# Kernel optimization log

Hardware: AMD Instinct MI355X
Metric: run time of the kernel (lower is better)

Reference implementation:

```python
import jax, jax.numpy as jnp
import numpy as np

B, N, Z = 32, 8192, 1024


def setup_inputs() -> dict:
    key = jax.random.key(0)
    ks = jax.random.split(key, 11)
    def w(k, shape, fan_in):
        # kaiming-ish init scale for conv1d k=1
        return jax.random.normal(k, shape, dtype=jnp.float32) * (1.0 / np.sqrt(fan_in))
    return {
        "x": jax.random.normal(ks[0], (B, 3, N), dtype=jnp.float32),
        "W1": w(ks[1], (64, 3), 3),   "b1": jnp.zeros((64,), jnp.float32),
        "W2": w(ks[2], (128, 64), 64), "b2": jnp.zeros((128,), jnp.float32),
        "W3": w(ks[3], (256, 128), 128), "b3": jnp.zeros((256,), jnp.float32),
        "W4": w(ks[4], (256, 256), 256), "b4": jnp.zeros((256,), jnp.float32),
        "W5": w(ks[5], (Z, 256), 256),  "b5": jnp.zeros((Z,), jnp.float32),
    }


def _pointwise(x, W, b):
    # Conv1d with kernel_size=1 == per-point linear: [B,C,N] x [O,C] -> [B,O,N]
    return jnp.einsum('bcn,oc->bon', x, W) + b[None, :, None]


def reference(x, W1, b1, W2, b2, W3, b3, W4, b4, W5, b5):
    h = jax.nn.relu(_pointwise(x, W1, b1))
    h = jax.nn.relu(_pointwise(h, W2, b2))
    h = jax.nn.relu(_pointwise(h, W3, b3))
    h = jax.nn.relu(_pointwise(h, W4, b4))
    h = _pointwise(h, W5, b5)           # [B, Z, N]
    return jnp.max(h, axis=2)           # global max pool over points -> [B, Z]
```

## Files before the change

### kernel.cpp

```cpp
#include <hip/hip_runtime.h>
#include <math.h>

#define NB      32
#define NPTS    8192
#define TOTPTS  (NB * NPTS)

typedef unsigned short u16;
typedef unsigned int   u32;
typedef __attribute__((ext_vector_type(8))) short bf16x8;
typedef __attribute__((ext_vector_type(4))) float f32x4;

__device__ __forceinline__ u16 f2bf(float f) {
    u32 u = __float_as_uint(f);
    u = (u + 0x7fffu + ((u >> 16) & 1u)) >> 16;
    return (u16)u;
}
__device__ __forceinline__ u32 pk2(float a, float b) {
    return (u32)f2bf(a) | ((u32)f2bf(b) << 16);
}
__device__ __forceinline__ f32x4 MFMA(bf16x8 a, bf16x8 b, f32x4 c) {
    return __builtin_amdgcn_mfma_f32_16x16x32_bf16(a, b, c, 0, 0, 0);
}
template<int CTRL>
__device__ __forceinline__ float dpp_max(float v) {
    int t = __builtin_amdgcn_update_dpp(__float_as_int(v), __float_as_int(v),
                                        CTRL, 0xF, 0xF, false);
    return fmaxf(v, __int_as_float(t));
}
__device__ __forceinline__ float rowmax16(float v) {
    v = dpp_max<0xB1>(v);
    v = dpp_max<0x4E>(v);
    v = dpp_max<0x141>(v);
    v = dpp_max<0x140>(v);
    return v;
}
__device__ __forceinline__ void gload16(const void* g, void* l) {
    __builtin_amdgcn_global_load_lds(
        (const __attribute__((address_space(1))) unsigned int*)g,
        (__attribute__((address_space(3))) unsigned int*)l, 16, 0, 0);
}
template<int N> __device__ __forceinline__ void vwait() {
    if constexpr (N == 0) asm volatile("s_waitcnt vmcnt(0)" ::: "memory");
    else                  asm volatile("s_waitcnt vmcnt(4)" ::: "memory");
}
__device__ __forceinline__ void pin(bf16x8& v)  { asm volatile("" : "+v"(v)); }
__device__ __forceinline__ void pinA(bf16x8& v) { asm volatile("" : "+a"(v)); }


__global__ __launch_bounds__(256) void k_pack(const float* __restrict__ W2,
        const float* __restrict__ W3, const float* __restrict__ W4,
        const float* __restrict__ W5, u16* __restrict__ dst) {
    int idx = blockIdx.x * 256 + threadIdx.x;
    if (idx >= 720 * 64) return;
    int lane = idx & 63, fr = idx >> 6;
    const float* W; int C, frl;
    if (fr < 16)       { W = W2; C = 64;  frl = fr;       }
    else if (fr < 80)  { W = W3; C = 128; frl = fr - 16;  }
    else if (fr < 208) { W = W4; C = 256; frl = fr - 80;  }
    else               { W = W5; C = 256; frl = fr - 208; }
    int KF = C >> 5;
    int nf = frl / KF, kf = frl % KF;
    int o = nf * 16 + (lane & 15), c = kf * 32 + (lane >> 4) * 8;
    const float* s = W + (size_t)o * C + c;
    u32 out[4];
    #pragma unroll
    for (int j = 0; j < 4; ++j) out[j] = pk2(s[2 * j], s[2 * j + 1]);
    *(uint4*)((char*)dst + (size_t)idx * 16) = make_uint4(out[0], out[1], out[2], out[3]);
}

__global__ __launch_bounds__(512, 2) void k_fuse(const float* __restrict__ x,
        const float* __restrict__ W1, const float* __restrict__ b1,
        const u16* __restrict__ W2p, const float* __restrict__ b2,
        const u16* __restrict__ W3p, const float* __restrict__ b3,
        const u16* __restrict__ W4p, const float* __restrict__ b4,
        u16* __restrict__ H4, int pt0, int tpb) {
    __shared__ char regA[65536];
    __shared__ char regB[32768];
    const int tid = threadIdx.x, lane = tid & 63, w = tid >> 6;
    const int l15 = lane & 15, q = lane >> 4;
    const int qterm = ((q >> 1) * 16 + l15) * 16 + (q & 1) * 8;
    const int pl = tid & 127;
    const int c4 = tid >> 7;

    bf16x8 W2r[2], W3r[2][4], W4r[2][8];
    #pragma unroll
    for (int kf = 0; kf < 2; ++kf) {
        W2r[kf] = *(const bf16x8*)((const char*)W2p + (size_t)(w * 2 + kf) * 1024 + lane * 16);
        pin(W2r[kf]);
    }
    #pragma unroll
    for (int n = 0; n < 2; ++n)
        #pragma unroll
        for (int kf = 0; kf < 4; ++kf) {
            W3r[n][kf] = *(const bf16x8*)((const char*)W3p +
                           (size_t)((w * 2 + n) * 4 + kf) * 1024 + lane * 16);
            pin(W3r[n][kf]);
        }
    #pragma unroll
    for (int n = 0; n < 2; ++n)
        #pragma unroll
        for (int kf = 0; kf < 8; ++kf) {
            W4r[n][kf] = *(const bf16x8*)((const char*)W4p +
                           (size_t)((w * 2 + n) * 8 + kf) * 1024 + lane * 16);
            pin(W4r[n][kf]);
        }
    const f32x4 b2v = *(const f32x4*)(b2 + w * 16 + q * 4);
    f32x4 b3v[2], b4v[2];
    #pragma unroll
    for (int n = 0; n < 2; ++n) {
        b3v[n] = *(const f32x4*)(b3 + (w * 2 + n) * 16 + q * 4);
        b4v[n] = *(const f32x4*)(b4 + (w * 2 + n) * 16 + q * 4);
    }

    const int tile0 = blockIdx.x * tpb;
    float x0, x1, x2;
    {
        int ptg = pt0 + tile0 * 128 + pl;
        const float* xb = x + (size_t)(ptg >> 13) * 3 * NPTS + (ptg & 8191);
        x0 = xb[0]; x1 = xb[NPTS]; x2 = xb[2 * NPTS];
    }

    for (int it = 0; it < tpb; ++it) {
        const int tile = tile0 + it;
        {
            u32 pk4[8];
            #pragma unroll
            for (int i = 0; i < 8; ++i) {
                int o0 = c4 * 16 + 2 * i, o1 = o0 + 1;
                float a0 = fmaxf(b1[o0] + W1[o0*3]*x0 + W1[o0*3+1]*x1 + W1[o0*3+2]*x2, 0.f);
                float a1 = fmaxf(b1[o1] + W1[o1*3]*x0 + W1[o1*3+1]*x1 + W1[o1*3+2]*x2, 0.f);
                pk4[i] = pk2(a0, a1);
            }
            char* rowp = regA + pl * 128;
            const int swz = (pl & 7) << 4;
            *(uint4*)(rowp + ((c4 * 32) ^ swz))      = make_uint4(pk4[0], pk4[1], pk4[2], pk4[3]);
            *(uint4*)(rowp + ((c4 * 32 + 16) ^ swz)) = make_uint4(pk4[4], pk4[5], pk4[6], pk4[7]);
        }
        __syncthreads();
        #pragma unroll
        for (int pf = 0; pf < 8; ++pf) {
            const int r2 = pf * 16 + l15;
            const char* rb = regA + r2 * 128;
            const int rsw = (r2 & 7) << 4;
            bf16x8 B0 = *(const bf16x8*)(rb + ((q * 16) ^ rsw));
            bf16x8 B1 = *(const bf16x8*)(rb + ((64 + q * 16) ^ rsw));
            f32x4 a = b2v;
            a = MFMA(W2r[0], B0, a);
            a = MFMA(W2r[1], B1, a);
            u32 d0 = pk2(fmaxf(a[0], 0.f), fmaxf(a[1], 0.f));
            u32 d1 = pk2(fmaxf(a[2], 0.f), fmaxf(a[3], 0.f));
            *(uint2*)(regB + (pf * 4 + (w >> 1)) * 1024 + (w & 1) * 512 + qterm)
                = make_uint2(d0, d1);
        }
        __syncthreads();
        #pragma unroll
        for (int pf = 0; pf < 8; ++pf) {
            bf16x8 B[4];
            #pragma unroll
            for (int kf = 0; kf < 4; ++kf)
                B[kf] = *(const bf16x8*)(regB + (pf * 4 + kf) * 1024 + lane * 16);
            f32x4 a0 = b3v[0], a1 = b3v[1];
            #pragma unroll
            for (int kf = 0; kf < 4; ++kf) {
                a0 = MFMA(W3r[0][kf], B[kf], a0);
                a1 = MFMA(W3r[1][kf], B[kf], a1);
            }
            char* db = regA + (pf * 8 + w) * 1024;
            *(uint2*)(db + qterm)       = make_uint2(pk2(fmaxf(a0[0],0.f), fmaxf(a0[1],0.f)),
                                                     pk2(fmaxf(a0[2],0.f), fmaxf(a0[3],0.f)));
            *(uint2*)(db + 512 + qterm) = make_uint2(pk2(fmaxf(a1[0],0.f), fmaxf(a1[1],0.f)),
                                                     pk2(fmaxf(a1[2],0.f), fmaxf(a1[3],0.f)));
        }
        __syncthreads();
        #pragma unroll
        for (int pf = 0; pf < 8; ++pf) {
            bf16x8 B[8];
            #pragma unroll
            for (int kf = 0; kf < 8; ++kf)
                B[kf] = *(const bf16x8*)(regA + (pf * 8 + kf) * 1024 + lane * 16);
            f32x4 a0 = b4v[0], a1 = b4v[1];
            #pragma unroll
            for (int kf = 0; kf < 8; ++kf) {
                a0 = MFMA(W4r[0][kf], B[kf], a0);
                a1 = MFMA(W4r[1][kf], B[kf], a1);
            }
            char* db = (char*)H4 + ((size_t)(tile * 8 + pf) * 8 + w) * 1024;
            *(uint2*)(db + qterm)       = make_uint2(pk2(fmaxf(a0[0],0.f), fmaxf(a0[1],0.f)),
                                                     pk2(fmaxf(a0[2],0.f), fmaxf(a0[3],0.f)));
            *(uint2*)(db + 512 + qterm) = make_uint2(pk2(fmaxf(a1[0],0.f), fmaxf(a1[1],0.f)),
                                                     pk2(fmaxf(a1[2],0.f), fmaxf(a1[3],0.f)));
        }
        if (it + 1 < tpb) {
            int ptg = pt0 + (tile + 1) * 128 + pl;
            const float* xb = x + (size_t)(ptg >> 13) * 3 * NPTS + (ptg & 8191);
            x0 = xb[0]; x1 = xb[NPTS]; x2 = xb[2 * NPTS];
        }
        __syncthreads();
    }
}

__global__ __launch_bounds__(512, 2) void k_l5(const u16* __restrict__ Hin,
        const u16* __restrict__ Wp, const float* __restrict__ b5,
        float* __restrict__ parts, int slot0) {
    constexpr int BUFB = 32768;
    constexpr int STEPS = 16;
    __shared__ char ldsB[2 * BUFB];
    const int tid = threadIdx.x, lane = tid & 63, w = tid >> 6;
    const int l15 = lane & 15, q = lane >> 4;
    const int zsl = blockIdx.x & 1, pgrp = blockIdx.x >> 1;
    const int pfb = pgrp * 64;

    bf16x8 W[4][8];
    {
        const char* wb = (const char*)Wp + (size_t)(zsl * 32 + w * 4) * 8 * 1024;
        #pragma unroll
        for (int nf = 0; nf < 4; ++nf)
            #pragma unroll
            for (int kf = 0; kf < 8; ++kf)
                W[nf][kf] = *(const bf16x8*)(wb + (size_t)(nf * 8 + kf) * 1024 + lane * 16);
    }
    f32x4 vmax[4];
    #pragma unroll
    for (int nf = 0; nf < 4; ++nf)
        #pragma unroll
        for (int r = 0; r < 4; ++r) vmax[nf][r] = -3.402823466e38f;

    auto stage = [&](int t, int bsel) {
        const char* g = (const char*)Hin + ((size_t)(pfb + t * 4) * 8) * 1024
                        + w * 4096 + lane * 16;
        char* l = ldsB + bsel * BUFB + w * 4096;
        gload16(g,        l);
        gload16(g + 1024, l + 1024);
        gload16(g + 2048, l + 2048);
        gload16(g + 3072, l + 3072);
    };
    stage(0, 0);
    for (int t = 0; t < STEPS; ++t) {
        vwait<0>();
        __builtin_amdgcn_sched_barrier(0);
        __builtin_amdgcn_s_barrier();
        if (t + 1 < STEPS) stage(t + 1, (t + 1) & 1);
        const char* bp = ldsB + (t & 1) * BUFB;
        #pragma unroll
        for (int p = 0; p < 4; ++p) {
            const int pe = (p + w) & 3;
            f32x4 acc[4];
            #pragma unroll
            for (int nf = 0; nf < 4; ++nf)
                #pragma unroll
                for (int r = 0; r < 4; ++r) acc[nf][r] = 0.f;
            #pragma unroll
            for (int kf = 0; kf < 8; ++kf) {
                bf16x8 B = *(const bf16x8*)(bp + (size_t)(pe * 8 + kf) * 1024 + lane * 16);
                #pragma unroll
                for (int nf = 0; nf < 4; ++nf) acc[nf] = MFMA(W[nf][kf], B, acc[nf]);
            }
            #pragma unroll
            for (int nf = 0; nf < 4; ++nf)
                #pragma unroll
                for (int r = 0; r < 4; ++r)
                    vmax[nf][r] = fmaxf(vmax[nf][r], acc[nf][r]);
        }
    }
    const int zb = zsl * 512 + w * 64;
    float* dst = parts + (size_t)(slot0 + pgrp) * 1024 + zb;
    #pragma unroll
    for (int nf = 0; nf < 4; ++nf)
        #pragma unroll
        for (int r = 0; r < 4; ++r) {
            float m = rowmax16(vmax[nf][r]);
            if (l15 == nf * 4 + r) {
                int zi = nf * 16 + q * 4 + r;
                dst[zi] = m + b5[zb + zi];
            }
        }
}

__global__ __launch_bounds__(256) void k_red(const float* __restrict__ parts,
                                             float* __restrict__ out) {
    int i = blockIdx.x * 256 + threadIdx.x;
    int b = i >> 10, z = i & 1023;
    float m = -3.402823466e38f;
    #pragma unroll
    for (int s = 0; s < 8; ++s)
        m = fmaxf(m, parts[((size_t)b * 8 + s) * 1024 + z]);
    out[i] = m;
}

extern "C" void kernel_launch(void* const* d_in, const int* in_sizes, int n_in,
                              void* d_out, int out_size, void* d_ws, size_t ws_size,
                              hipStream_t stream) {
    const float* x  = (const float*)d_in[0];
    const float* W1 = (const float*)d_in[1]; const float* b1 = (const float*)d_in[2];
    const float* W2 = (const float*)d_in[3]; const float* b2 = (const float*)d_in[4];
    const float* W3 = (const float*)d_in[5]; const float* b3 = (const float*)d_in[6];
    const float* W4 = (const float*)d_in[7]; const float* b4 = (const float*)d_in[8];
    const float* W5 = (const float*)d_in[9]; const float* b5 = (const float*)d_in[10];

    u16* wsW = (u16*)d_ws;
    const u16* W2p = (const u16*)((char*)d_ws + 0);
    const u16* W3p = (const u16*)((char*)d_ws + 16 * 1024);
    const u16* W4p = (const u16*)((char*)d_ws + 80 * 1024);
    const u16* W5p = (const u16*)((char*)d_ws + 208 * 1024);
    float* parts   = (float*)((char*)d_ws + 786432);
    char* Hbase    = (char*)d_ws + 786432 + 2097152;

    int NCH = 1;
    while (NCH < 32) {
        size_t npc = (size_t)TOTPTS / NCH;
        if (786432 + 2097152 + npc * 512 <= ws_size) break;
        NCH *= 2;
    }
    const size_t npts_c = (size_t)TOTPTS / NCH;
    char* HB = Hbase;

    k_pack<<<dim3(180), dim3(256), 0, stream>>>(W2, W3, W4, W5, wsW);

    const int ntiles = (int)(npts_c / 128);
    const int nblk   = (ntiles >= 256) ? 256 : ntiles;
    const int tpb    = ntiles / nblk;
    for (int c = 0; c < NCH; ++c) {
        int pt0   = (int)(c * npts_c);
        int slot0 = (int)((c * npts_c) >> 10);
        k_fuse<<<dim3(nblk), dim3(512), 0, stream>>>(
            x, W1, b1, W2p, b2, W3p, b3, W4p, b4, (u16*)HB, pt0, tpb);
        k_l5<<<dim3(2 * (int)(npts_c / 1024)), dim3(512), 0, stream>>>(
            (const u16*)HB, W5p, b5, parts, slot0);
    }
    k_red<<<dim3(128), dim3(256), 0, stream>>>(parts, (float*)d_out);
}
```

Baseline: 166.6 us.

## Load layer-5 activations directly to registers with double buffering instead of LDS staging

The final layer kernel no longer stages activation fragments through shared memory with global_load_lds and block barriers. Each wave now reads its B fragments straight from global memory into registers, alternating between two register sets so the next point-fragment's loads overlap the current MFMA chain. Weights are pinned in accumulator registers to free VGPRs for the two buffers. This removes LDS round-trips and block-wide syncs. In exchange, every wave independently reads all 64 point fragments (8x more global/L2 traffic per block), and register pressure rises.

```diff
diff --git a/kernel.cpp b/kernel.cpp
--- a/kernel.cpp
+++ b/kernel.cpp
@@ -33,15 +33,6 @@
     v = dpp_max<0x141>(v);
     v = dpp_max<0x140>(v);
     return v;
-}
-__device__ __forceinline__ void gload16(const void* g, void* l) {
-    __builtin_amdgcn_global_load_lds(
-        (const __attribute__((address_space(1))) unsigned int*)g,
-        (__attribute__((address_space(3))) unsigned int*)l, 16, 0, 0);
-}
-template<int N> __device__ __forceinline__ void vwait() {
-    if constexpr (N == 0) asm volatile("s_waitcnt vmcnt(0)" ::: "memory");
-    else                  asm volatile("s_waitcnt vmcnt(4)" ::: "memory");
 }
 __device__ __forceinline__ void pin(bf16x8& v)  { asm volatile("" : "+v"(v)); }
 __device__ __forceinline__ void pinA(bf16x8& v) { asm volatile("" : "+a"(v)); }
@@ -202,9 +193,6 @@
 __global__ __launch_bounds__(512, 2) void k_l5(const u16* __restrict__ Hin,
         const u16* __restrict__ Wp, const float* __restrict__ b5,
         float* __restrict__ parts, int slot0) {
-    constexpr int BUFB = 32768;
-    constexpr int STEPS = 16;
-    __shared__ char ldsB[2 * BUFB];
     const int tid = threadIdx.x, lane = tid & 63, w = tid >> 6;
     const int l15 = lane & 15, q = lane >> 4;
     const int zsl = blockIdx.x & 1, pgrp = blockIdx.x >> 1;
@@ -216,8 +204,10 @@
         #pragma unroll
         for (int nf = 0; nf < 4; ++nf)
             #pragma unroll
-            for (int kf = 0; kf < 8; ++kf)
+            for (int kf = 0; kf < 8; ++kf) {
                 W[nf][kf] = *(const bf16x8*)(wb + (size_t)(nf * 8 + kf) * 1024 + lane * 16);
+                pinA(W[nf][kf]);
+            }
     }
     f32x4 vmax[4];
     #pragma unroll
@@ -225,36 +215,52 @@
         #pragma unroll
         for (int r = 0; r < 4; ++r) vmax[nf][r] = -3.402823466e38f;
 
-    auto stage = [&](int t, int bsel) {
-        const char* g = (const char*)Hin + ((size_t)(pfb + t * 4) * 8) * 1024
-                        + w * 4096 + lane * 16;
-        char* l = ldsB + bsel * BUFB + w * 4096;
-        gload16(g,        l);
-        gload16(g + 1024, l + 1024);
-        gload16(g + 2048, l + 2048);
-        gload16(g + 3072, l + 3072);
-    };
-    stage(0, 0);
-    for (int t = 0; t < STEPS; ++t) {
-        vwait<0>();
-        __builtin_amdgcn_sched_barrier(0);
-        __builtin_amdgcn_s_barrier();
-        if (t + 1 < STEPS) stage(t + 1, (t + 1) & 1);
-        const char* bp = ldsB + (t & 1) * BUFB;
-        #pragma unroll
-        for (int p = 0; p < 4; ++p) {
-            const int pe = (p + w) & 3;
+    const char* g0 = (const char*)Hin + (size_t)pfb * 8192 + lane * 16;
+
+    bf16x8 Ba[8], Bb[8];
+    #pragma unroll
+    for (int kf = 0; kf < 8; ++kf)
+        Ba[kf] = *(const bf16x8*)(g0 + kf * 1024);
+
+    for (int t = 0; t < 64; t += 2) {
+        {
+            const char* g1 = g0 + (size_t)(t + 1) * 8192;
+            #pragma unroll
+            for (int kf = 0; kf < 8; ++kf)
+                Bb[kf] = *(const bf16x8*)(g1 + kf * 1024);
+        }
+        {
             f32x4 acc[4];
             #pragma unroll
             for (int nf = 0; nf < 4; ++nf)
                 #pragma unroll
                 for (int r = 0; r < 4; ++r) acc[nf][r] = 0.f;
             #pragma unroll
-            for (int kf = 0; kf < 8; ++kf) {
-                bf16x8 B = *(const bf16x8*)(bp + (size_t)(pe * 8 + kf) * 1024 + lane * 16);
-                #pragma unroll
-                for (int nf = 0; nf < 4; ++nf) acc[nf] = MFMA(W[nf][kf], B, acc[nf]);
-            }
+            for (int kf = 0; kf < 8; ++kf)
+                #pragma unroll
+                for (int nf = 0; nf < 4; ++nf) acc[nf] = MFMA(W[nf][kf], Ba[kf], acc[nf]);
+            #pragma unroll
+            for (int nf = 0; nf < 4; ++nf)
+                #pragma unroll
+                for (int r = 0; r < 4; ++r)
+                    vmax[nf][r] = fmaxf(vmax[nf][r], acc[nf][r]);
+        }
+        if (t + 2 < 64) {
+            const char* g2 = g0 + (size_t)(t + 2) * 8192;
+            #pragma unroll
+            for (int kf = 0; kf < 8; ++kf)
+                Ba[kf] = *(const bf16x8*)(g2 + kf * 1024);
+        }
+        {
+            f32x4 acc[4];
+            #pragma unroll
+            for (int nf = 0; nf < 4; ++nf)
+                #pragma unroll
+                for (int r = 0; r < 4; ++r) acc[nf][r] = 0.f;
+            #pragma unroll
+            for (int kf = 0; kf < 8; ++kf)
+                #pragma unroll
+                for (int nf = 0; nf < 4; ++nf) acc[nf] = MFMA(W[nf][kf], Bb[kf], acc[nf]);
             #pragma unroll
             for (int nf = 0; nf < 4; ++nf)
                 #pragma unroll
```

New measurement: 190.5 us. 14.4% more time.
